# Kernel optimization log

Measured on AMD Instinct MI355X. Metric: run time of the kernel, lower is better.

Reference implementation:

```python
import jax, jax.numpy as jnp
import numpy as np

N = 100000   # nodes
E = 3200000  # edges (avg degree 32)
F = 128      # node_features
H = 128      # GCN hidden
A = 1024     # num_actions
B = 256      # graphs in batch


def setup_inputs() -> dict:
    key = jax.random.key(0)
    ks = jax.random.split(key, 11)
    glorot = lambda k, shp: (jax.random.normal(k, shp, jnp.float32)
                             / np.sqrt(float(shp[0])))
    return {
        "x": jax.random.normal(ks[0], (N, F), jnp.float32),
        "edge_index": jax.random.randint(ks[1], (2, E), 0, N, dtype=jnp.int64),
        "batch": jnp.sort(jax.random.randint(ks[2], (N,), 0, B, dtype=jnp.int64)),
        "W1": glorot(ks[3], (F, H)), "b1": jnp.zeros((H,), jnp.float32),
        "W2": glorot(ks[4], (H, H)), "b2": jnp.zeros((H,), jnp.float32),
        "Wv": glorot(ks[5], (H, 1)), "bv": jnp.zeros((1,), jnp.float32),
        "Wp": glorot(ks[6], (H, A)), "bp": jnp.zeros((A,), jnp.float32),
    }


def reference(x, edge_index, batch, W1, b1, W2, b2, Wv, bv, Wp, bp):
    # --- GCN normalization (PyG gcn_norm with self-loops) ---
    loops = jnp.arange(N, dtype=edge_index.dtype)
    src = jnp.concatenate([edge_index[0], loops])  # [E+N] message sources
    dst = jnp.concatenate([edge_index[1], loops])  # [E+N] aggregation targets
    deg = jax.ops.segment_sum(jnp.ones(src.shape, jnp.float32), dst,
                              num_segments=N)       # in-degree incl. self-loop
    dinv = jax.lax.rsqrt(deg)                       # deg >= 1 due to self-loops
    norm = (dinv[src] * dinv[dst])[:, None]         # [E+N, 1]

    def gcn_conv(h, W, b):
        h = h @ W                                   # transform first (small GEMM)
        agg = jax.ops.segment_sum(h[src] * norm, dst, num_segments=N)
        return agg + b

    h = jax.nn.relu(gcn_conv(x, W1, b1))
    h = jax.nn.relu(gcn_conv(h, W2, b2))

    # --- global_mean_pool over graph ids ---
    counts = jax.ops.segment_sum(jnp.ones((N,), jnp.float32), batch,
                                 num_segments=B)
    pooled = jax.ops.segment_sum(h, batch, num_segments=B) \
             / jnp.maximum(counts, 1.0)[:, None]    # [B, H]

    v = jnp.tanh(pooled @ Wv + bv)                  # [B, 1]
    p = jax.nn.softmax(pooled @ Wp + bp, axis=-1)   # [B, A]
    return (v, p)
```

## Files before the change

### kernel.cpp

```cpp
#include <hip/hip_runtime.h>
#include <hip/hip_bf16.h>

#define GN 100000
#define GE 3200000
#define GH 128
#define GA 1024
#define GB 256

#define NBUK 391
#define B1BLK 5120
#define NBIN1 625

typedef __attribute__((ext_vector_type(8))) short short8v;
typedef __attribute__((ext_vector_type(4))) float f32x4v;

__device__ __forceinline__ unsigned int f2bf(float f) {
    unsigned int u = __float_as_uint(f);
    return (u + 0x7fffu + ((u >> 16) & 1u)) >> 16;
}
__device__ __forceinline__ float bflo(unsigned int u) { return __uint_as_float(u << 16); }
__device__ __forceinline__ float bfhi(unsigned int u) { return __uint_as_float(u & 0xffff0000u); }


__global__ __launch_bounds__(256) void k_hist_coarse(const int* __restrict__ dst,
                                                     int* __restrict__ cnt) {
    __shared__ int h[NBUK];
    int t = threadIdx.x;
    for (int i = t; i < NBUK; i += 256) h[i] = 0;
    __syncthreads();
    int beg = blockIdx.x * 3125;
    for (int e = beg + t; e < beg + 3125; e += 256)
        atomicAdd(&h[dst[e] >> 8], 1);
    __syncthreads();
    for (int i = t; i < NBUK; i += 256) {
        int c = h[i];
        if (c) atomicAdd(&cnt[i], c);
    }
}

__global__ __launch_bounds__(256) void k_scan_coarse(const int* __restrict__ cnt,
                                                     int* __restrict__ gcur,
                                                     int* __restrict__ cbase,
                                                     int* __restrict__ offsets) {
    __shared__ int wsc[4];
    int t = threadIdx.x;
    int i0 = 2 * t, i1 = 2 * t + 1;
    int v0 = (i0 < NBUK) ? cnt[i0] : 0;
    int v1 = (i1 < NBUK) ? cnt[i1] : 0;
    int s = v0 + v1;
    int lane = t & 63, w = t >> 6;
    int x = s;
#pragma unroll
    for (int off = 1; off < 64; off <<= 1) {
        int y = __shfl_up(x, off);
        if (lane >= off) x += y;
    }
    if (lane == 63) wsc[w] = x;
    __syncthreads();
    int wo = 0;
#pragma unroll
    for (int i = 0; i < 4; i++)
        if (i < w) wo += wsc[i];
    int excl = wo + x - s;
    if (i0 < NBUK) { cbase[i0] = excl; gcur[i0] = excl; }
    if (i1 < NBUK) { cbase[i1] = excl + v0; gcur[i1] = excl + v0; }
    if (t == 0) { cbase[NBUK] = GE; offsets[GN] = GE; }
}

__global__ __launch_bounds__(256) void k_bin1(const int* __restrict__ src,
                                              const int* __restrict__ dst,
                                              int* __restrict__ gcur,
                                              unsigned int* __restrict__ binned) {
    __shared__ int hist[512], lstart[512];
    __shared__ int curl[NBUK], gbase[NBUK];
    __shared__ unsigned int srec[B1BLK];
    __shared__ unsigned short sbuk[B1BLK];
    __shared__ int wsc[4];
    int t = threadIdx.x;
    hist[t] = 0; hist[t + 256] = 0;
    __syncthreads();
    int beg = blockIdx.x * B1BLK;
    unsigned int rec[20]; int bukv[20];
#pragma unroll
    for (int k = 0; k < 20; k++) {
        int e = beg + t + k * 256;
        int d = dst[e];
        rec[k] = (unsigned int)src[e] | ((unsigned int)(d & 255) << 17);
        bukv[k] = d >> 8;
        atomicAdd(&hist[bukv[k]], 1);
    }
    __syncthreads();
    int v0 = hist[2 * t], v1 = hist[2 * t + 1];
    int s = v0 + v1;
    int lane = t & 63, w = t >> 6;
    int x = s;
#pragma unroll
    for (int off = 1; off < 64; off <<= 1) {
        int y = __shfl_up(x, off);
        if (lane >= off) x += y;
    }
    if (lane == 63) wsc[w] = x;
    __syncthreads();
    int wo = 0;
#pragma unroll
    for (int i = 0; i < 4; i++)
        if (i < w) wo += wsc[i];
    int excl = wo + x - s;
    lstart[2 * t] = excl;
    lstart[2 * t + 1] = excl + v0;
    __syncthreads();
    for (int i = t; i < NBUK; i += 256) {
        curl[i] = lstart[i];
        int c = hist[i];
        gbase[i] = c ? atomicAdd(&gcur[i], c) : 0;
    }
    __syncthreads();
#pragma unroll
    for (int k = 0; k < 20; k++) {
        int p = atomicAdd(&curl[bukv[k]], 1);
        srec[p] = rec[k];
        sbuk[p] = (unsigned short)bukv[k];
    }
    __syncthreads();
    for (int i = t; i < B1BLK; i += 256) {
        int b = sbuk[i];
        binned[gbase[b] + (i - lstart[b])] = srec[i];
    }
}

__global__ __launch_bounds__(256) void k_sort2(const unsigned int* __restrict__ binned,
                                               const int* __restrict__ cbase,
                                               int* __restrict__ csr_src,
                                               int* __restrict__ offsets,
                                               float* __restrict__ dinv) {
    int b = blockIdx.x, t = threadIdx.x;
    __shared__ int hist[256], cur[256], wsum[4];
    hist[t] = 0;
    __syncthreads();
    int rbase = cbase[b], rend = cbase[b + 1];
    for (int e = rbase + t; e < rend; e += 256)
        atomicAdd(&hist[(binned[e] >> 17) & 255], 1);
    __syncthreads();
    int h = hist[t];
    int lane = t & 63, w = t >> 6;
    int x = h;
#pragma unroll
    for (int off = 1; off < 64; off <<= 1) {
        int y = __shfl_up(x, off);
        if (lane >= off) x += y;
    }
    if (lane == 63) wsum[w] = x;
    __syncthreads();
    int wo = 0;
#pragma unroll
    for (int i = 0; i < 4; i++)
        if (i < w) wo += wsum[i];
    int excl = wo + x - h;
    int node = (b << 8) + t;
    if (node < GN) {
        offsets[node] = rbase + excl;
        dinv[node] = rsqrtf((float)(h + 1));
    }
    cur[t] = excl;
    __syncthreads();
    for (int e = rbase + t; e < rend; e += 256) {
        unsigned int v = binned[e];
        int dl = (v >> 17) & 255;
        int p = atomicAdd(&cur[dl], 1);
        csr_src[rbase + p] = (int)(v & 0x1FFFF);
    }
}

__global__ __launch_bounds__(256) void k_cvt(const float* __restrict__ x,
                                             unsigned int* __restrict__ xb) {
    size_t i = (size_t)blockIdx.x * 256 + threadIdx.x;
    if (i < (size_t)GN * 64) {
        float2 v = ((const float2*)x)[i];
        xb[i] = f2bf(v.x) | (f2bf(v.y) << 16);
    }
}

__global__ __launch_bounds__(256) void k_gemm_mfma(const unsigned int* __restrict__ A,
                                                   const float* __restrict__ W,
                                                   const float* __restrict__ dinv,
                                                   unsigned int* __restrict__ C) {
    __shared__ unsigned short Wf[16384];
    __shared__ float Ct[64][128];
    int t = threadIdx.x;
    int row0 = blockIdx.x * 64;
    for (int i = 0; i < 64; i++) {
        int idx = t + 256 * i;
        int k = idx >> 7, n = idx & 127;
        int qd = (((k >> 5) * 8 + (n >> 4)) * 64 + ((k >> 3) & 3) * 16 + (n & 15)) * 8 + (k & 7);
        Wf[qd] = (unsigned short)f2bf(W[idx]);
    }
    __syncthreads();
    int wv = t >> 6, lane = t & 63;
    int m16 = lane & 15, g = lane >> 4;
    f32x4v acc[8];
#pragma unroll
    for (int nb = 0; nb < 8; nb++) acc[nb] = (f32x4v){0.f, 0.f, 0.f, 0.f};
    int arow = row0 + wv * 16 + m16; if (arow >= GN) arow = GN - 1;
#pragma unroll
    for (int kb = 0; kb < 4; kb++) {
        uint4 av = *(const uint4*)&A[(size_t)arow * 64 + kb * 16 + g * 4];
        short8v af = *(short8v*)&av;
#pragma unroll
        for (int nb = 0; nb < 8; nb++) {
            short8v bf = *(short8v*)&Wf[((kb * 8 + nb) * 64 + lane) * 8];
            acc[nb] = __builtin_amdgcn_mfma_f32_16x16x32_bf16(af, bf, acc[nb], 0, 0, 0);
        }
    }
#pragma unroll
    for (int nb = 0; nb < 8; nb++)
#pragma unroll
        for (int r = 0; r < 4; r++)
            Ct[wv * 16 + g * 4 + r][nb * 16 + m16] = acc[nb][r];
    __syncthreads();
    int lr = t >> 2, ch = t & 3;
    int grow = row0 + lr;
    if (grow < GN) {
        float dv = dinv[grow];
#pragma unroll
        for (int q = 0; q < 4; q++) {
            int c0 = ch * 32 + q * 8;
            uint4 po;
            po.x = f2bf(Ct[lr][c0 + 0] * dv) | (f2bf(Ct[lr][c0 + 1] * dv) << 16);
            po.y = f2bf(Ct[lr][c0 + 2] * dv) | (f2bf(Ct[lr][c0 + 3] * dv) << 16);
            po.z = f2bf(Ct[lr][c0 + 4] * dv) | (f2bf(Ct[lr][c0 + 5] * dv) << 16);
            po.w = f2bf(Ct[lr][c0 + 6] * dv) | (f2bf(Ct[lr][c0 + 7] * dv) << 16);
            *(uint4*)&C[(size_t)grow * 64 + ch * 16 + q * 4] = po;
        }
    }
}

__global__ __launch_bounds__(256) void k_aggregate(const unsigned int* __restrict__ ts,
                                                   const int* __restrict__ offsets,
                                                   const int* __restrict__ csr_src,
                                                   const float* __restrict__ dinv,
                                                   const float* __restrict__ bias,
                                                   unsigned int* __restrict__ out) {
    int node = blockIdx.x * 4 + (threadIdx.x >> 6);
    if (node >= GN) return;
    int lane = threadIdx.x & 63;
    int beg = offsets[node];
    int end = offsets[node + 1];
    float di = dinv[node];
    float ax = 0.f, ay = 0.f;
    for (int base = beg; base < end; base += 64) {
        int n = end - base; if (n > 64) n = 64;
        int myidx = (lane < n) ? csr_src[base + lane] : 0;
        int k = 0;
        for (; k + 16 <= n; k += 16) {
            unsigned int u[16];
#pragma unroll
            for (int q = 0; q < 16; q++) {
                int s = __shfl(myidx, k + q);
                u[q] = ts[s * 64 + lane];
            }
#pragma unroll
            for (int q = 0; q < 16; q++) { ax += bflo(u[q]); ay += bfhi(u[q]); }
        }
        for (; k + 4 <= n; k += 4) {
            unsigned int u[4];
#pragma unroll
            for (int q = 0; q < 4; q++) {
                int s = __shfl(myidx, k + q);
                u[q] = ts[s * 64 + lane];
            }
#pragma unroll
            for (int q = 0; q < 4; q++) { ax += bflo(u[q]); ay += bfhi(u[q]); }
        }
        for (; k < n; k++) {
            int s = __shfl(myidx, k);
            unsigned int u = ts[s * 64 + lane];
            ax += bflo(u); ay += bfhi(u);
        }
    }
    unsigned int su = ts[(size_t)node * 64 + lane];
    float bx = bias[lane * 2 + 0], by = bias[lane * 2 + 1];
    float ox = fmaxf(fmaf(di, ax + bflo(su), bx), 0.f);
    float oy = fmaxf(fmaf(di, ay + bfhi(su), by), 0.f);
    out[(size_t)node * 64 + lane] = f2bf(ox) | (f2bf(oy) << 16);
}

__global__ __launch_bounds__(256) void k_pool(const unsigned int* __restrict__ h,
                                              const int* __restrict__ batch,
                                              float* __restrict__ pooled) {
    int g = blockIdx.x;
    int t = threadIdx.x;
    int f = t & 63, part = t >> 6;
    int lo = 0, hi = GN;
    while (lo < hi) { int m = (lo + hi) >> 1; if (batch[m] < g) lo = m + 1; else hi = m; }
    int start = lo;
    hi = GN;
    while (lo < hi) { int m = (lo + hi) >> 1; if (batch[m] <= g) lo = m + 1; else hi = m; }
    int end = lo;
    float ax = 0.f, ay = 0.f;
    for (int i = start + part; i < end; i += 4) {
        unsigned int u = h[(size_t)i * 64 + f];
        ax += bflo(u); ay += bfhi(u);
    }
    __shared__ float redx[256], redy[256];
    redx[t] = ax; redy[t] = ay;
    __syncthreads();
    if (part == 0) {
        float sx = redx[f] + redx[f + 64] + redx[f + 128] + redx[f + 192];
        float sy = redy[f] + redy[f + 64] + redy[f + 128] + redy[f + 192];
        float inv = 1.0f / fmaxf((float)(end - start), 1.0f);
        pooled[g * 128 + 2 * f + 0] = sx * inv;
        pooled[g * 128 + 2 * f + 1] = sy * inv;
    }
}

__global__ void k_value(const float* __restrict__ pooled, const float* __restrict__ Wv,
                        const float* __restrict__ bv, float* __restrict__ out) {
    int g = threadIdx.x;
    const float4* p4 = (const float4*)(pooled + g * 128);
    const float4* w4 = (const float4*)Wv;
    float s = 0.f;
#pragma unroll 8
    for (int i = 0; i < 32; i++) {
        float4 a = p4[i], b = w4[i];
        s += a.x * b.x + a.y * b.y + a.z * b.z + a.w * b.w;
    }
    out[g] = tanhf(s + bv[0]);
}

__global__ __launch_bounds__(256) void k_policy(const float* __restrict__ pooled,
                                                const float* __restrict__ Wp,
                                                const float* __restrict__ bp,
                                                float* __restrict__ out) {
    int g = blockIdx.x;
    int t = threadIdx.x;
    __shared__ float pr[128];
    __shared__ float red[256];
    if (t < 128) pr[t] = pooled[g * 128 + t];
    __syncthreads();
    float acc0 = bp[t + 0], acc1 = bp[t + 256], acc2 = bp[t + 512], acc3 = bp[t + 768];
    for (int k = 0; k < 128; k++) {
        float pv = pr[k];
        const float* wr = Wp + (size_t)k * 1024;
        acc0 = fmaf(pv, wr[t + 0],   acc0);
        acc1 = fmaf(pv, wr[t + 256], acc1);
        acc2 = fmaf(pv, wr[t + 512], acc2);
        acc3 = fmaf(pv, wr[t + 768], acc3);
    }
    float m = fmaxf(fmaxf(acc0, acc1), fmaxf(acc2, acc3));
    red[t] = m;
    __syncthreads();
    for (int off = 128; off > 0; off >>= 1) {
        if (t < off) red[t] = fmaxf(red[t], red[t + off]);
        __syncthreads();
    }
    float mx = red[0];
    __syncthreads();
    float e0 = __expf(acc0 - mx), e1 = __expf(acc1 - mx);
    float e2 = __expf(acc2 - mx), e3 = __expf(acc3 - mx);
    red[t] = (e0 + e1) + (e2 + e3);
    __syncthreads();
    for (int off = 128; off > 0; off >>= 1) {
        if (t < off) red[t] += red[t + off];
        __syncthreads();
    }
    float inv = 1.0f / red[0];
    out[(size_t)g * 1024 + t + 0]   = e0 * inv;
    out[(size_t)g * 1024 + t + 256] = e1 * inv;
    out[(size_t)g * 1024 + t + 512] = e2 * inv;
    out[(size_t)g * 1024 + t + 768] = e3 * inv;
}

extern "C" void kernel_launch(void* const* d_in, const int* in_sizes, int n_in,
                              void* d_out, int out_size, void* d_ws, size_t ws_size,
                              hipStream_t stream) {
    const float* x    = (const float*)d_in[0];
    const int*   ei   = (const int*)d_in[1];
    const int*   srcA = ei;
    const int*   dstA = ei + GE;
    const int*   batch = (const int*)d_in[2];
    const float* W1 = (const float*)d_in[3];
    const float* b1 = (const float*)d_in[4];
    const float* W2 = (const float*)d_in[5];
    const float* b2 = (const float*)d_in[6];
    const float* Wv = (const float*)d_in[7];
    const float* bv = (const float*)d_in[8];
    const float* Wp = (const float*)d_in[9];
    const float* bp = (const float*)d_in[10];
    float* out = (float*)d_out;

    char* ws = (char*)d_ws;
    unsigned int* bufH = (unsigned int*)ws;  ws += (size_t)GN * 64 * 4;
    unsigned int* ts_bf = (unsigned int*)ws; ws += (size_t)GN * 64 * 4;
    unsigned int* xbf = (unsigned int*)ws;   ws += (size_t)GN * 64 * 4;
    float* pooled = (float*)ws;      ws += (size_t)GB * 128 * 4;
    float* dinv = (float*)ws;        ws += (size_t)100352 * 4;
    int*   csr_src = (int*)ws;       ws += (size_t)GE * 4;
    int*   offsets = (int*)ws;       ws += (size_t)100352 * 4;
    int*   coarse_cnt = (int*)ws;    ws += 512 * 4;
    int*   gcur = (int*)ws;          ws += 512 * 4;
    int*   cbase = (int*)ws;         ws += 512 * 4;
    unsigned int* binned = ts_bf;

    hipMemsetAsync(coarse_cnt, 0, NBUK * 4, stream);
    k_cvt<<<(GN * 64 + 255) / 256, 256, 0, stream>>>(x, xbf);
    k_hist_coarse<<<1024, 256, 0, stream>>>(dstA, coarse_cnt);
    k_scan_coarse<<<1, 256, 0, stream>>>(coarse_cnt, gcur, cbase, offsets);
    k_bin1<<<NBIN1, 256, 0, stream>>>(srcA, dstA, gcur, binned);
    k_sort2<<<NBUK, 256, 0, stream>>>(binned, cbase, csr_src, offsets, dinv);

    k_gemm_mfma<<<(GN + 63) / 64, 256, 0, stream>>>(xbf, W1, dinv, ts_bf);
    k_aggregate<<<GN / 4, 256, 0, stream>>>(ts_bf, offsets, csr_src, dinv, b1, bufH);

    k_gemm_mfma<<<(GN + 63) / 64, 256, 0, stream>>>(bufH, W2, dinv, ts_bf);
    k_aggregate<<<GN / 4, 256, 0, stream>>>(ts_bf, offsets, csr_src, dinv, b2, bufH);

    k_pool<<<GB, 256, 0, stream>>>(bufH, batch, pooled);
    k_value<<<1, 256, 0, stream>>>(pooled, Wv, bv, out);
    k_policy<<<GB, 256, 0, stream>>>(pooled, Wp, bp, out + GB);
}
```

Measured before the change: 427.6 us.

## Drop coarse histogram pass, fuse x conversion into GEMM1, pre-swizzle weights, batch policy

Replaces the coarse destination histogram and scan with fixed-capacity buckets. Each bucket now starts at i*BCAP, and per-node begin/end arrays are stored instead of a contiguous offsets array. The separate fp32-to-bf16 conversion pass over x is folded into the first GEMM's A-operand load. The weight swizzle and bf16 conversion move into a one-time prep kernel instead of being redone by every GEMM block. The policy head now processes four graphs per block so each Wp row load is reused. The fixed bucket capacity assumes no bucket exceeds 12288 edges, which holds for roughly uniform destinations but would overflow on skewed graphs.

```diff
diff --git a/kernel.cpp b/kernel.cpp
--- a/kernel.cpp
+++ b/kernel.cpp
@@ -8,6 +8,7 @@
 #define GB 256
 
 #define NBUK 391
+#define BCAP 12288
 #define B1BLK 5120
 #define NBIN1 625
 
@@ -21,50 +22,27 @@
 __device__ __forceinline__ float bflo(unsigned int u) { return __uint_as_float(u << 16); }
 __device__ __forceinline__ float bfhi(unsigned int u) { return __uint_as_float(u & 0xffff0000u); }
 
-
-__global__ __launch_bounds__(256) void k_hist_coarse(const int* __restrict__ dst,
-                                                     int* __restrict__ cnt) {
-    __shared__ int h[NBUK];
-    int t = threadIdx.x;
-    for (int i = t; i < NBUK; i += 256) h[i] = 0;
-    __syncthreads();
-    int beg = blockIdx.x * 3125;
-    for (int e = beg + t; e < beg + 3125; e += 256)
-        atomicAdd(&h[dst[e] >> 8], 1);
-    __syncthreads();
-    for (int i = t; i < NBUK; i += 256) {
-        int c = h[i];
-        if (c) atomicAdd(&cnt[i], c);
-    }
-}
-
-__global__ __launch_bounds__(256) void k_scan_coarse(const int* __restrict__ cnt,
-                                                     int* __restrict__ gcur,
-                                                     int* __restrict__ cbase,
-                                                     int* __restrict__ offsets) {
-    __shared__ int wsc[4];
-    int t = threadIdx.x;
-    int i0 = 2 * t, i1 = 2 * t + 1;
-    int v0 = (i0 < NBUK) ? cnt[i0] : 0;
-    int v1 = (i1 < NBUK) ? cnt[i1] : 0;
-    int s = v0 + v1;
-    int lane = t & 63, w = t >> 6;
-    int x = s;
-#pragma unroll
-    for (int off = 1; off < 64; off <<= 1) {
-        int y = __shfl_up(x, off);
-        if (lane >= off) x += y;
-    }
-    if (lane == 63) wsc[w] = x;
-    __syncthreads();
-    int wo = 0;
-#pragma unroll
-    for (int i = 0; i < 4; i++)
-        if (i < w) wo += wsc[i];
-    int excl = wo + x - s;
-    if (i0 < NBUK) { cbase[i0] = excl; gcur[i0] = excl; }
-    if (i1 < NBUK) { cbase[i1] = excl + v0; gcur[i1] = excl + v0; }
-    if (t == 0) { cbase[NBUK] = GE; offsets[GN] = GE; }
+__device__ __forceinline__ int wswz(int k, int n) {
+    return (((k >> 5) * 8 + (n >> 4)) * 64 + ((k >> 3) & 3) * 16 + (n & 15)) * 8 + (k & 7);
+}
+
+__global__ __launch_bounds__(256) void k_prep(const float* __restrict__ W1,
+                                              const float* __restrict__ W2,
+                                              unsigned short* __restrict__ Wsw1,
+                                              unsigned short* __restrict__ Wsw2,
+                                              int* __restrict__ gcur) {
+    int b = blockIdx.x, t = threadIdx.x;
+    if (b < 64) {
+        int idx = b * 256 + t;
+        int k = idx >> 7, n = idx & 127;
+        Wsw1[wswz(k, n)] = (unsigned short)f2bf(W1[idx]);
+    } else if (b < 128) {
+        int idx = (b - 64) * 256 + t;
+        int k = idx >> 7, n = idx & 127;
+        Wsw2[wswz(k, n)] = (unsigned short)f2bf(W2[idx]);
+    } else {
+        for (int i = t; i < NBUK; i += 256) gcur[i] = i * BCAP;
+    }
 }
 
 __global__ __launch_bounds__(256) void k_bin1(const int* __restrict__ src,
@@ -129,15 +107,17 @@
 }
 
 __global__ __launch_bounds__(256) void k_sort2(const unsigned int* __restrict__ binned,
-                                               const int* __restrict__ cbase,
+                                               const int* __restrict__ gcur,
                                                int* __restrict__ csr_src,
-                                               int* __restrict__ offsets,
+                                               int* __restrict__ nbeg,
+                                               int* __restrict__ nend,
                                                float* __restrict__ dinv) {
     int b = blockIdx.x, t = threadIdx.x;
     __shared__ int hist[256], cur[256], wsum[4];
     hist[t] = 0;
     __syncthreads();
-    int rbase = cbase[b], rend = cbase[b + 1];
+    int rbase = b * BCAP;
+    int rend = gcur[b];
     for (int e = rbase + t; e < rend; e += 256)
         atomicAdd(&hist[(binned[e] >> 17) & 255], 1);
     __syncthreads();
@@ -158,7 +138,8 @@
     int excl = wo + x - h;
     int node = (b << 8) + t;
     if (node < GN) {
-        offsets[node] = rbase + excl;
+        nbeg[node] = rbase + excl;
+        nend[node] = rbase + excl + h;
         dinv[node] = rsqrtf((float)(h + 1));
     }
     cur[t] = excl;
@@ -171,30 +152,13 @@
     }
 }
 
-__global__ __launch_bounds__(256) void k_cvt(const float* __restrict__ x,
-                                             unsigned int* __restrict__ xb) {
-    size_t i = (size_t)blockIdx.x * 256 + threadIdx.x;
-    if (i < (size_t)GN * 64) {
-        float2 v = ((const float2*)x)[i];
-        xb[i] = f2bf(v.x) | (f2bf(v.y) << 16);
-    }
-}
-
-__global__ __launch_bounds__(256) void k_gemm_mfma(const unsigned int* __restrict__ A,
-                                                   const float* __restrict__ W,
-                                                   const float* __restrict__ dinv,
-                                                   unsigned int* __restrict__ C) {
-    __shared__ unsigned short Wf[16384];
+__global__ __launch_bounds__(256) void k_gemm1(const float* __restrict__ A,
+                                               const unsigned short* __restrict__ Wsw,
+                                               const float* __restrict__ dinv,
+                                               unsigned int* __restrict__ C) {
     __shared__ float Ct[64][128];
     int t = threadIdx.x;
     int row0 = blockIdx.x * 64;
-    for (int i = 0; i < 64; i++) {
-        int idx = t + 256 * i;
-        int k = idx >> 7, n = idx & 127;
-        int qd = (((k >> 5) * 8 + (n >> 4)) * 64 + ((k >> 3) & 3) * 16 + (n & 15)) * 8 + (k & 7);
-        Wf[qd] = (unsigned short)f2bf(W[idx]);
-    }
-    __syncthreads();
     int wv = t >> 6, lane = t & 63;
     int m16 = lane & 15, g = lane >> 4;
     f32x4v acc[8];
@@ -203,11 +167,18 @@
     int arow = row0 + wv * 16 + m16; if (arow >= GN) arow = GN - 1;
 #pragma unroll
     for (int kb = 0; kb < 4; kb++) {
-        uint4 av = *(const uint4*)&A[(size_t)arow * 64 + kb * 16 + g * 4];
-        short8v af = *(short8v*)&av;
+        const float* ap = &A[(size_t)arow * 128 + kb * 32 + g * 8];
+        float4 a0 = *(const float4*)ap;
+        float4 a1 = *(const float4*)(ap + 4);
+        uint4 up;
+        up.x = f2bf(a0.x) | (f2bf(a0.y) << 16);
+        up.y = f2bf(a0.z) | (f2bf(a0.w) << 16);
+        up.z = f2bf(a1.x) | (f2bf(a1.y) << 16);
+        up.w = f2bf(a1.z) | (f2bf(a1.w) << 16);
+        short8v af = *(short8v*)&up;
 #pragma unroll
         for (int nb = 0; nb < 8; nb++) {
-            short8v bf = *(short8v*)&Wf[((kb * 8 + nb) * 64 + lane) * 8];
+            short8v bf = *(const short8v*)&Wsw[((kb * 8 + nb) * 64 + lane) * 8];
             acc[nb] = __builtin_amdgcn_mfma_f32_16x16x32_bf16(af, bf, acc[nb], 0, 0, 0);
         }
     }
@@ -234,8 +205,55 @@
     }
 }
 
+__global__ __launch_bounds__(256) void k_gemm2(const unsigned int* __restrict__ A,
+                                               const unsigned short* __restrict__ Wsw,
+                                               const float* __restrict__ dinv,
+                                               unsigned int* __restrict__ C) {
+    __shared__ float Ct[64][128];
+    int t = threadIdx.x;
+    int row0 = blockIdx.x * 64;
+    int wv = t >> 6, lane = t & 63;
+    int m16 = lane & 15, g = lane >> 4;
+    f32x4v acc[8];
+#pragma unroll
+    for (int nb = 0; nb < 8; nb++) acc[nb] = (f32x4v){0.f, 0.f, 0.f, 0.f};
+    int arow = row0 + wv * 16 + m16; if (arow >= GN) arow = GN - 1;
+#pragma unroll
+    for (int kb = 0; kb < 4; kb++) {
+        uint4 av = *(const uint4*)&A[(size_t)arow * 64 + kb * 16 + g * 4];
+        short8v af = *(short8v*)&av;
+#pragma unroll
+        for (int nb = 0; nb < 8; nb++) {
+            short8v bf = *(const short8v*)&Wsw[((kb * 8 + nb) * 64 + lane) * 8];
+            acc[nb] = __builtin_amdgcn_mfma_f32_16x16x32_bf16(af, bf, acc[nb], 0, 0, 0);
+        }
+    }
+#pragma unroll
+    for (int nb = 0; nb < 8; nb++)
+#pragma unroll
+        for (int r = 0; r < 4; r++)
+            Ct[wv * 16 + g * 4 + r][nb * 16 + m16] = acc[nb][r];
+    __syncthreads();
+    int lr = t >> 2, ch = t & 3;
+    int grow = row0 + lr;
+    if (grow < GN) {
+        float dv = dinv[grow];
+#pragma unroll
+        for (int q = 0; q < 4; q++) {
+            int c0 = ch * 32 + q * 8;
+            uint4 po;
+            po.x = f2bf(Ct[lr][c0 + 0] * dv) | (f2bf(Ct[lr][c0 + 1] * dv) << 16);
+            po.y = f2bf(Ct[lr][c0 + 2] * dv) | (f2bf(Ct[lr][c0 + 3] * dv) << 16);
+            po.z = f2bf(Ct[lr][c0 + 4] * dv) | (f2bf(Ct[lr][c0 + 5] * dv) << 16);
+            po.w = f2bf(Ct[lr][c0 + 6] * dv) | (f2bf(Ct[lr][c0 + 7] * dv) << 16);
+            *(uint4*)&C[(size_t)grow * 64 + ch * 16 + q * 4] = po;
+        }
+    }
+}
+
 __global__ __launch_bounds__(256) void k_aggregate(const unsigned int* __restrict__ ts,
-                                                   const int* __restrict__ offsets,
+                                                   const int* __restrict__ nbeg,
+                                                   const int* __restrict__ nend,
                                                    const int* __restrict__ csr_src,
                                                    const float* __restrict__ dinv,
                                                    const float* __restrict__ bias,
@@ -243,8 +261,8 @@
     int node = blockIdx.x * 4 + (threadIdx.x >> 6);
     if (node >= GN) return;
     int lane = threadIdx.x & 63;
-    int beg = offsets[node];
-    int end = offsets[node + 1];
+    int beg = nbeg[node];
+    int end = nend[node];
     float di = dinv[node];
     float ax = 0.f, ay = 0.f;
     for (int base = beg; base < end; base += 64) {
@@ -331,43 +349,61 @@
                                                 const float* __restrict__ Wp,
                                                 const float* __restrict__ bp,
                                                 float* __restrict__ out) {
-    int g = blockIdx.x;
+    int g0 = blockIdx.x * 4;
     int t = threadIdx.x;
-    __shared__ float pr[128];
+    __shared__ float pr[4][128];
     __shared__ float red[256];
-    if (t < 128) pr[t] = pooled[g * 128 + t];
-    __syncthreads();
-    float acc0 = bp[t + 0], acc1 = bp[t + 256], acc2 = bp[t + 512], acc3 = bp[t + 768];
+    if (t < 128) {
+#pragma unroll
+        for (int gg = 0; gg < 4; gg++)
+            pr[gg][t] = pooled[(size_t)(g0 + gg) * 128 + t];
+    }
+    __syncthreads();
+    float bb0 = bp[t], bb1 = bp[t + 256], bb2 = bp[t + 512], bb3 = bp[t + 768];
+    float acc[4][4];
+#pragma unroll
+    for (int gg = 0; gg < 4; gg++) {
+        acc[gg][0] = bb0; acc[gg][1] = bb1; acc[gg][2] = bb2; acc[gg][3] = bb3;
+    }
     for (int k = 0; k < 128; k++) {
-        float pv = pr[k];
         const float* wr = Wp + (size_t)k * 1024;
-        acc0 = fmaf(pv, wr[t + 0],   acc0);
-        acc1 = fmaf(pv, wr[t + 256], acc1);
-        acc2 = fmaf(pv, wr[t + 512], acc2);
-        acc3 = fmaf(pv, wr[t + 768], acc3);
-    }
-    float m = fmaxf(fmaxf(acc0, acc1), fmaxf(acc2, acc3));
-    red[t] = m;
-    __syncthreads();
-    for (int off = 128; off > 0; off >>= 1) {
-        if (t < off) red[t] = fmaxf(red[t], red[t + off]);
+        float w0 = wr[t], w1 = wr[t + 256], w2 = wr[t + 512], w3 = wr[t + 768];
+#pragma unroll
+        for (int gg = 0; gg < 4; gg++) {
+            float pv = pr[gg][k];
+            acc[gg][0] = fmaf(pv, w0, acc[gg][0]);
+            acc[gg][1] = fmaf(pv, w1, acc[gg][1]);
+            acc[gg][2] = fmaf(pv, w2, acc[gg][2]);
+            acc[gg][3] = fmaf(pv, w3, acc[gg][3]);
+        }
+    }
+#pragma unroll
+    for (int gg = 0; gg < 4; gg++) {
+        float m = fmaxf(fmaxf(acc[gg][0], acc[gg][1]), fmaxf(acc[gg][2], acc[gg][3]));
+        red[t] = m;
         __syncthreads();
-    }
-    float mx = red[0];
-    __syncthreads();
-    float e0 = __expf(acc0 - mx), e1 = __expf(acc1 - mx);
-    float e2 = __expf(acc2 - mx), e3 = __expf(acc3 - mx);
-    red[t] = (e0 + e1) + (e2 + e3);
-    __syncthreads();
-    for (int off = 128; off > 0; off >>= 1) {
-        if (t < off) red[t] += red[t + off];
+        for (int off = 128; off > 0; off >>= 1) {
+            if (t < off) red[t] = fmaxf(red[t], red[t + off]);
+            __syncthreads();
+        }
+        float mx = red[0];
         __syncthreads();
-    }
-    float inv = 1.0f / red[0];
-    out[(size_t)g * 1024 + t + 0]   = e0 * inv;
-    out[(size_t)g * 1024 + t + 256] = e1 * inv;
-    out[(size_t)g * 1024 + t + 512] = e2 * inv;
-    out[(size_t)g * 1024 + t + 768] = e3 * inv;
+        float e0 = __expf(acc[gg][0] - mx), e1 = __expf(acc[gg][1] - mx);
+        float e2 = __expf(acc[gg][2] - mx), e3 = __expf(acc[gg][3] - mx);
+        red[t] = (e0 + e1) + (e2 + e3);
+        __syncthreads();
+        for (int off = 128; off > 0; off >>= 1) {
+            if (t < off) red[t] += red[t + off];
+            __syncthreads();
+        }
+        float inv = 1.0f / red[0];
+        __syncthreads();
+        size_t ob = (size_t)(g0 + gg) * 1024;
+        out[ob + t + 0]   = e0 * inv;
+        out[ob + t + 256] = e1 * inv;
+        out[ob + t + 512] = e2 * inv;
+        out[ob + t + 768] = e3 * inv;
+    }
 }
 
 extern "C" void kernel_launch(void* const* d_in, const int* in_sizes, int n_in,
@@ -391,30 +427,27 @@
     char* ws = (char*)d_ws;
     unsigned int* bufH = (unsigned int*)ws;  ws += (size_t)GN * 64 * 4;
     unsigned int* ts_bf = (unsigned int*)ws; ws += (size_t)GN * 64 * 4;
-    unsigned int* xbf = (unsigned int*)ws;   ws += (size_t)GN * 64 * 4;
     float* pooled = (float*)ws;      ws += (size_t)GB * 128 * 4;
     float* dinv = (float*)ws;        ws += (size_t)100352 * 4;
-    int*   csr_src = (int*)ws;       ws += (size_t)GE * 4;
-    int*   offsets = (int*)ws;       ws += (size_t)100352 * 4;
-    int*   coarse_cnt = (int*)ws;    ws += 512 * 4;
+    int*   nbeg = (int*)ws;          ws += (size_t)100352 * 4;
+    int*   nend = (int*)ws;          ws += (size_t)100352 * 4;
+    int*   csr_src = (int*)ws;       ws += (size_t)NBUK * BCAP * 4;
     int*   gcur = (int*)ws;          ws += 512 * 4;
-    int*   cbase = (int*)ws;         ws += 512 * 4;
+    unsigned short* Wsw1 = (unsigned short*)ws; ws += 16384 * 2;
+    unsigned short* Wsw2 = (unsigned short*)ws; ws += 16384 * 2;
     unsigned int* binned = ts_bf;
 
-    hipMemsetAsync(coarse_cnt, 0, NBUK * 4, stream);
-    k_cvt<<<(GN * 64 + 255) / 256, 256, 0, stream>>>(x, xbf);
-    k_hist_coarse<<<1024, 256, 0, stream>>>(dstA, coarse_cnt);
-    k_scan_coarse<<<1, 256, 0, stream>>>(coarse_cnt, gcur, cbase, offsets);
+    k_prep<<<129, 256, 0, stream>>>(W1, W2, Wsw1, Wsw2, gcur);
     k_bin1<<<NBIN1, 256, 0, stream>>>(srcA, dstA, gcur, binned);
-    k_sort2<<<NBUK, 256, 0, stream>>>(binned, cbase, csr_src, offsets, dinv);
-
-    k_gemm_mfma<<<(GN + 63) / 64, 256, 0, stream>>>(xbf, W1, dinv, ts_bf);
-    k_aggregate<<<GN / 4, 256, 0, stream>>>(ts_bf, offsets, csr_src, dinv, b1, bufH);
-
-    k_gemm_mfma<<<(GN + 63) / 64, 256, 0, stream>>>(bufH, W2, dinv, ts_bf);
-    k_aggregate<<<GN / 4, 256, 0, stream>>>(ts_bf, offsets, csr_src, dinv, b2, bufH);
+    k_sort2<<<NBUK, 256, 0, stream>>>(binned, gcur, csr_src, nbeg, nend, dinv);
+
+    k_gemm1<<<(GN + 63) / 64, 256, 0, stream>>>(x, Wsw1, dinv, ts_bf);
+    k_aggregate<<<GN / 4, 256, 0, stream>>>(ts_bf, nbeg, nend, csr_src, dinv, b1, bufH);
+
+    k_gemm2<<<(GN + 63) / 64, 256, 0, stream>>>(bufH, Wsw2, dinv, ts_bf);
+    k_aggregate<<<GN / 4, 256, 0, stream>>>(ts_bf, nbeg, nend, csr_src, dinv, b2, bufH);
 
     k_pool<<<GB, 256, 0, stream>>>(bufH, batch, pooled);
     k_value<<<1, 256, 0, stream>>>(pooled, Wv, bv, out);
-    k_policy<<<GB, 256, 0, stream>>>(pooled, Wp, bp, out + GB);
-}
+    k_policy<<<GB / 4, 256, 0, stream>>>(pooled, Wp, bp, out + GB);
+}
```

Result: faster. 372.8 us (-12.8%).
